# Kernel tuning notes

Measured on AMD Instinct MI355X. Metric: run time of the kernel, lower is better.

## Reference

```python
import jax, jax.numpy as jnp
import numpy as np

K = 20
EPS = 1e-5
NEG_SLOPE = 0.2


def knn(x, k):
    # x: [B, C, N] -> idx [B, N, k] of nearest neighbors (negative sq-dist topk)
    inner = -2.0 * jnp.einsum('bcn,bcm->bnm', x, x)
    xx = jnp.sum(x * x, axis=1)  # [B, N]
    d = -xx[:, :, None] - inner - xx[:, None, :]
    return jax.lax.top_k(d, k)[1]


def get_graph_feature(x, k):
    # x: [B, C, N] -> [B, 2C, N, k]
    idx = knn(x, k)
    xt = jnp.transpose(x, (0, 2, 1))            # [B, N, C]
    feat = jax.vmap(lambda a, i: a[i])(xt, idx)  # [B, N, k, C]
    center = xt[:, :, None, :]
    out = jnp.concatenate([feat - center, jnp.broadcast_to(center, feat.shape)], axis=-1)
    return jnp.transpose(out, (0, 3, 1, 2))


def conv_bn_lrelu(x, w, g, b):
    # 1x1 conv + BatchNorm2d (batch stats, training mode) + LeakyReLU(0.2)
    y = jnp.einsum('oc,bcnk->bonk', w, x)
    mu = jnp.mean(y, axis=(0, 2, 3), keepdims=True)
    var = jnp.mean((y - mu) ** 2, axis=(0, 2, 3), keepdims=True)
    y = (y - mu) * jax.lax.rsqrt(var + EPS)
    y = y * g[None, :, None, None] + b[None, :, None, None]
    return jnp.where(y >= 0, y, NEG_SLOPE * y)


def lrelu(y):
    return jnp.where(y >= 0, y, NEG_SLOPE * y)


def setup_inputs() -> dict:
    key = jax.random.key(0)
    ks = jax.random.split(key, 24)
    B, N = 8, 4096
    d = {}
    d['x'] = jax.random.normal(ks[0], (B, 3, N), dtype=jnp.float32)
    def wconv(k_, o, c):
        return jax.random.normal(k_, (o, c), dtype=jnp.float32) * (1.0 / np.sqrt(c))
    d['w1'] = wconv(ks[1], 32, 6)
    d['g1'] = 1.0 + 0.1 * jax.random.normal(ks[2], (32,), dtype=jnp.float32)
    d['b1'] = 0.1 * jax.random.normal(ks[3], (32,), dtype=jnp.float32)
    d['w2'] = wconv(ks[4], 64, 70)
    d['g2'] = 1.0 + 0.1 * jax.random.normal(ks[5], (64,), dtype=jnp.float32)
    d['b2'] = 0.1 * jax.random.normal(ks[6], (64,), dtype=jnp.float32)
    d['wd1'] = wconv(ks[7], 64, 64)
    d['gd1'] = 1.0 + 0.1 * jax.random.normal(ks[8], (64,), dtype=jnp.float32)
    d['bd1'] = 0.1 * jax.random.normal(ks[9], (64,), dtype=jnp.float32)
    d['wd2'] = wconv(ks[10], 64, 128)
    d['gd2'] = 1.0 + 0.1 * jax.random.normal(ks[11], (64,), dtype=jnp.float32)
    d['bd2'] = 0.1 * jax.random.normal(ks[12], (64,), dtype=jnp.float32)
    d['W2d'] = jax.random.normal(ks[13], (128, 128), dtype=jnp.float32) * (1.0 / np.sqrt(128))
    d['b2d'] = 0.1 * jax.random.normal(ks[14], (128,), dtype=jnp.float32)
    d['W3d'] = jax.random.normal(ks[15], (64, 128), dtype=jnp.float32) * (1.0 / np.sqrt(128))
    d['b3d'] = 0.1 * jax.random.normal(ks[16], (64,), dtype=jnp.float32)
    d['W4d'] = jax.random.normal(ks[17], (11, 64), dtype=jnp.float32) * (1.0 / np.sqrt(64))
    d['b4d'] = 0.1 * jax.random.normal(ks[18], (11,), dtype=jnp.float32)
    return d


def reference(x, w1, g1, b1, w2, g2, b2, wd1, gd1, bd1, wd2, gd2, bd2,
              W2d, b2d, W3d, b3d, W4d, b4d):
    x1_gf = get_graph_feature(x, K)                    # [B, 6, N, k]
    x1_max = jnp.max(conv_bn_lrelu(x1_gf, w1, g1, b1), axis=-1)  # [B, 32, N]
    x2_gf = jnp.concatenate([x1_gf, get_graph_feature(x1_max, K)], axis=1)  # [B, 70, N, k]
    x2_max = jnp.max(conv_bn_lrelu(x2_gf, w2, g2, b2), axis=-1)  # [B, 64, N]
    xd1 = jnp.max(conv_bn_lrelu(get_graph_feature(x1_max, K), wd1, gd1, bd1), axis=-1)  # [B, 64, N]
    xd2 = jnp.max(conv_bn_lrelu(get_graph_feature(x2_max, K), wd2, gd2, bd2), axis=-1)  # [B, 64, N]
    h = jnp.concatenate([xd1, xd2], axis=1)            # [B, 128, N]
    h = h.reshape(1, -1, 128)                          # faithful row-major view
    h = jnp.mean(h, axis=1)                            # [1, 128]
    h = lrelu(h @ W2d.T + b2d)
    h = lrelu(h @ W3d.T + b3d)
    return lrelu(h @ W4d.T + b4d)                      # [1, 11]
```

## Files before the change

### kernel.cpp

```cpp
#include <hip/hip_runtime.h>

#define BB 8
#define NN 4096
#define KK 20
constexpr float EPSV = 1e-5f;
constexpr float SLOPE = 0.2f;

typedef __bf16 bfrag __attribute__((ext_vector_type(8)));
typedef float floatx4 __attribute__((ext_vector_type(4)));
typedef unsigned short us8 __attribute__((ext_vector_type(8)));

__device__ __forceinline__ float lrelu(float v) { return v >= 0.f ? v : SLOPE * v; }

__device__ __forceinline__ unsigned short bf16rn(float f) {
    unsigned int u = __float_as_uint(f);
    return (unsigned short)((u + 0x7FFFu + ((u >> 16) & 1u)) >> 16);
}
__device__ __forceinline__ float bf16up(unsigned short h) {
    return __uint_as_float(((unsigned int)h) << 16);
}

__device__ __forceinline__ void gl2lds16(const void* g, void* l) {
    __builtin_amdgcn_global_load_lds(
        (const __attribute__((address_space(1))) unsigned int*)g,
        (__attribute__((address_space(3))) unsigned int*)l, 16, 0, 0);
}

__global__ void zero_kernel(float* p, int n) {
    int i = blockIdx.x * 256 + threadIdx.x;
    if (i < n) p[i] = 0.f;
}

template<int C>
__global__ void halfnorm_kernel(const float* __restrict__ src, float* __restrict__ hng) {
    int n = blockIdx.x * 256 + threadIdx.x;
    int b = blockIdx.y;
    float s = 0.f;
    #pragma unroll
    for (int c = 0; c < C; c++) { float v = src[(b * C + c) * NN + n]; s += v * v; }
    hng[b * NN + n] = 0.5f * s;
}

template<int C>
__global__ void pack_kernel(const float* __restrict__ src, unsigned short* __restrict__ pk) {
    constexpr int NCH = C / 4;
    int i = blockIdx.x * 256 + threadIdx.x;
    int b = blockIdx.y;
    int n = i / NCH, j = i % NCH;
    us8 v;
    if (j < C / 8) {
        int c0 = j * 8;
        #pragma unroll
        for (int cc = 0; cc < 8; cc++)
            v[cc] = bf16rn(src[(b * C + c0 + cc) * NN + n]);
    } else {
        int c0 = (j - C / 8) * 8;
        #pragma unroll
        for (int cc = 0; cc < 8; cc++) {
            float f = src[(b * C + c0 + cc) * NN + n];
            unsigned short h = bf16rn(f);
            v[cc] = bf16rn(f - bf16up(h));
        }
    }
    int phys = j ^ (n & (NCH - 1));
    *(us8*)(pk + ((size_t)(b * NN + n) * NCH + phys) * 8) = v;
}

__global__ void pack3_kernel(const float* __restrict__ src,
                             unsigned short* __restrict__ pa, unsigned short* __restrict__ pb) {
    int n = blockIdx.x * 256 + threadIdx.x;
    int b = blockIdx.y;
    unsigned short h[3], l[3];
    #pragma unroll
    for (int c = 0; c < 3; c++) {
        float f = src[(b * 3 + c) * NN + n];
        h[c] = bf16rn(f);
        l[c] = bf16rn(f - bf16up(h[c]));
    }
    unsigned short A[32], B[32];
    #pragma unroll
    for (int k = 0; k < 32; k++) { A[k] = 0; B[k] = 0; }
    #pragma unroll
    for (int c = 0; c < 3; c++) {
        A[c] = h[c];     A[3 + c] = l[c];  A[6 + c] = h[c];  A[9 + c] = l[c];
        B[c] = h[c];     B[3 + c] = l[c];  B[6 + c] = l[c];  B[9 + c] = h[c];
    }
    size_t base = (size_t)(b * NN + n) * 32;
    #pragma unroll
    for (int j = 0; j < 4; j++) {
        int phys = j ^ (n & 3);
        us8 va, vb;
        #pragma unroll
        for (int t = 0; t < 8; t++) { va[t] = A[j * 8 + t]; vb[t] = B[j * 8 + t]; }
        *(us8*)(pa + base + phys * 8) = va;
        *(us8*)(pb + base + phys * 8) = vb;
    }
}

template<int C>
__global__ __launch_bounds__(256) void knn_kernel(const unsigned short* __restrict__ pq,
                                                  const unsigned short* __restrict__ pc,
                                                  const float* __restrict__ hng,
                                                  int* __restrict__ idx) {
    constexpr int RS = (C == 3) ? 32 : 2 * C;
    constexpr int NCHR = RS / 8;
    constexpr int SWM = NCHR - 1;
    __shared__ unsigned short qpack[64 * RS];
    __shared__ unsigned short cpack[128 * RS];
    __shared__ float hn[128];
    __shared__ float pv[64 * 33];
    __shared__ unsigned short pidx[64 * 34];
    __shared__ float tau[64];
    __shared__ int   cnt[64];

    const int b = blockIdx.y;
    const int q0 = blockIdx.x * 64;
    const int tid = threadIdx.x;
    const int lane = tid & 63;
    const int wv = tid >> 6;
    const int fl = lane & 15;
    const int fq = lane >> 4;
    const int wr = (wv >> 1) * 32;
    const int wc = (wv & 1) * 64;

    {
        const char* gq = (const char*)(pq + (size_t)(b * NN + q0) * RS);
        constexpr int PQW = (64 * RS * 2 / 1024) / 4;
        #pragma unroll
        for (int t = 0; t < PQW; t++) {
            int seg = wv * PQW + t;
            gl2lds16(gq + seg * 1024 + lane * 16, (char*)qpack + seg * 1024);
        }
    }
    if (tid < 64) { tau[tid] = -3.4e38f; cnt[tid] = 0; }

    float tv[20]; int ti[20];
    #pragma unroll
    for (int k = 0; k < 20; k++) { tv[k] = -3.4e38f; ti[k] = 0; }

    for (int ch = 0; ch < 32; ch++) {
        const int m0 = ch * 128;
        {
            const char* gc = (const char*)(pc + (size_t)(b * NN + m0) * RS);
            constexpr int PCW = (128 * RS * 2 / 1024) / 4;
            #pragma unroll
            for (int t = 0; t < PCW; t++) {
                int seg = wv * PCW + t;
                gl2lds16(gc + seg * 1024 + lane * 16, (char*)cpack + seg * 1024);
            }
        }
        if (tid < 128) hn[tid] = hng[b * NN + m0 + tid];
        __syncthreads();

        floatx4 acc[2][4];
        #pragma unroll
        for (int r2 = 0; r2 < 2; r2++)
            #pragma unroll
            for (int c2 = 0; c2 < 4; c2++)
                acc[r2][c2] = (floatx4)(0.f);

        if constexpr (C == 3) {
            bfrag a[2];
            #pragma unroll
            for (int r2 = 0; r2 < 2; r2++) {
                int row = wr + r2 * 16 + fl;
                a[r2] = *(const bfrag*)(qpack + row * RS + (fq ^ (row & SWM)) * 8);
            }
            #pragma unroll
            for (int c2 = 0; c2 < 4; c2++) {
                int row = wc + c2 * 16 + fl;
                bfrag bm = *(const bfrag*)(cpack + row * RS + (fq ^ (row & SWM)) * 8);
                #pragma unroll
                for (int r2 = 0; r2 < 2; r2++)
                    acc[r2][c2] = __builtin_amdgcn_mfma_f32_16x16x32_bf16(a[r2], bm, acc[r2][c2], 0, 0, 0);
            }
        } else {
            #pragma unroll
            for (int kk = 0; kk < C / 32; kk++) {
                bfrag ah[2], al[2], bh[4], bl[4];
                #pragma unroll
                for (int r2 = 0; r2 < 2; r2++) {
                    int row = wr + r2 * 16 + fl;
                    ah[r2] = *(const bfrag*)(qpack + row * RS + ((kk * 4 + fq) ^ (row & SWM)) * 8);
                    al[r2] = *(const bfrag*)(qpack + row * RS + ((C / 8 + kk * 4 + fq) ^ (row & SWM)) * 8);
                }
                #pragma unroll
                for (int c2 = 0; c2 < 4; c2++) {
                    int row = wc + c2 * 16 + fl;
                    bh[c2] = *(const bfrag*)(cpack + row * RS + ((kk * 4 + fq) ^ (row & SWM)) * 8);
                    bl[c2] = *(const bfrag*)(cpack + row * RS + ((C / 8 + kk * 4 + fq) ^ (row & SWM)) * 8);
                }
                #pragma unroll
                for (int r2 = 0; r2 < 2; r2++)
                    #pragma unroll
                    for (int c2 = 0; c2 < 4; c2++) {
                        acc[r2][c2] = __builtin_amdgcn_mfma_f32_16x16x32_bf16(ah[r2], bh[c2], acc[r2][c2], 0, 0, 0);
                        acc[r2][c2] = __builtin_amdgcn_mfma_f32_16x16x32_bf16(ah[r2], bl[c2], acc[r2][c2], 0, 0, 0);
                        acc[r2][c2] = __builtin_amdgcn_mfma_f32_16x16x32_bf16(al[r2], bh[c2], acc[r2][c2], 0, 0, 0);
                        acc[r2][c2] = __builtin_amdgcn_mfma_f32_16x16x32_bf16(al[r2], bl[c2], acc[r2][c2], 0, 0, 0);
                    }
            }
        }

        auto filter_one = [&](int c2) {
            float hnv = hn[wc + c2 * 16 + fl];
            #pragma unroll
            for (int r2 = 0; r2 < 2; r2++) {
                const float* tp = &tau[wr + r2 * 16 + fq * 4];
                float t0 = tp[0], t1 = tp[1], t2 = tp[2], t3 = tp[3];
                float ta[4] = {t0, t1, t2, t3};
                #pragma unroll
                for (int reg = 0; reg < 4; reg++) {
                    float s = acc[r2][c2][reg] - hnv;
                    if (s > ta[reg]) {
                        int q = wr + r2 * 16 + fq * 4 + reg;
                        int p = atomicAdd(&cnt[q], 1);
                        if (p < 32) {
                            pv[q * 33 + p] = s;
                            pidx[q * 34 + p] = (unsigned short)(m0 + wc + c2 * 16 + fl);
                        }
                    }
                }
            }
        };
        auto drain = [&]() {
            if (lane < 16) {
                int qd = wv * 16 + lane;
                int n = cnt[qd]; if (n > 32) n = 32;
                for (int t = 0; t < n; t++) {
                    float v = pv[qd * 33 + t];
                    if (v > tv[0]) {
                        tv[0] = v; ti[0] = (int)pidx[qd * 34 + t];
                        #pragma unroll
                        for (int j = 0; j < 19; j++) {
                            if (tv[j] > tv[j + 1]) {
                                float a = tv[j]; tv[j] = tv[j + 1]; tv[j + 1] = a;
                                int bi = ti[j]; ti[j] = ti[j + 1]; ti[j + 1] = bi;
                            }
                        }
                    }
                }
                cnt[qd] = 0;
                tau[qd] = tv[0];
            }
        };

        if (ch == 0) {
            #pragma unroll
            for (int ph = 0; ph < 4; ph++) {
                filter_one(ph);
                __syncthreads();
                drain();
                __syncthreads();
            }
        } else {
            #pragma unroll
            for (int c2 = 0; c2 < 4; c2++) filter_one(c2);
            __syncthreads();
            drain();
        }
    }

    if (lane < 16) {
        int q = q0 + wv * 16 + lane;
        #pragma unroll
        for (int k = 0; k < 20; k++)
            idx[(b * NN + q) * KK + k] = ti[k];
    }
}

template<int COUT>
__global__ void precompute_kernel(const float* __restrict__ src, int C,
                                  const float* __restrict__ w, int CIN, int wd_off, int wc_off,
                                  float* __restrict__ G, float* __restrict__ H,
                                  int initG, int initH) {
    constexpr int MY = 256 / COUT;
    extern __shared__ float lds[];
    float* wd = lds;
    float* wc = lds + C * COUT;
    const int b = blockIdx.y;
    const int tid = threadIdx.y * COUT + threadIdx.x;
    for (int i = tid; i < C * COUT; i += 256) {
        int c = i / COUT, o = i % COUT;
        float a  = w[o * CIN + wd_off + c];
        float cc = w[o * CIN + wc_off + c];
        wd[i] = a;
        wc[i] = cc - a;
    }
    __syncthreads();
    const int o = threadIdx.x;
    for (int it = 0; it < COUT / 4; it++) {
        int m = blockIdx.x * 64 + it * MY + threadIdx.y;
        float g = 0.f, h = 0.f;
        for (int c = 0; c < C; c++) {
            float s = src[(b * C + c) * NN + m];
            g += wd[c * COUT + o] * s;
            h += wc[c * COUT + o] * s;
        }
        int gi = (b * NN + m) * COUT + o;
        if (initG) G[gi] = g; else G[gi] += g;
        if (initH) H[gi] = h; else H[gi] += h;
    }
}

template<int COUT, int GROUPS>
__global__ void conv_stats_kernel(const float* __restrict__ G1, const int* __restrict__ idx1,
                                  const float* __restrict__ G2, const int* __restrict__ idx2,
                                  const float* __restrict__ H, float* __restrict__ stats,
                                  float* __restrict__ MaxY, float* __restrict__ MinY) {
    constexpr int NY = 256 / COUT;
    const int b = blockIdx.y;
    const int o = threadIdx.x;
    const int n = blockIdx.x * NY + threadIdx.y;
    const int base = b * NN + n;
    const float h = H[base * COUT + o];
    float s1 = 0.f, s2 = 0.f;
    float gx = -3.4e38f, gn = 3.4e38f;
    #pragma unroll
    for (int k = 0; k < KK; k++) {
        int i1 = idx1[base * KK + k];
        float g = G1[(b * NN + i1) * COUT + o];
        if (GROUPS == 2) {
            int i2 = idx2[base * KK + k];
            g += G2[(b * NN + i2) * COUT + o];
        }
        float y = g + h;
        s1 += y;
        s2 += y * y;
        gx = fmaxf(gx, g);
        gn = fminf(gn, g);
    }
    MaxY[base * COUT + o] = gx + h;
    MinY[base * COUT + o] = gn + h;

    __shared__ float ls[2 * COUT];
    if (threadIdx.y == 0) { ls[o] = 0.f; ls[COUT + o] = 0.f; }
    __syncthreads();
    atomicAdd(&ls[o], s1);
    atomicAdd(&ls[COUT + o], s2);
    __syncthreads();
    if (threadIdx.y == 0) {
        atomicAdd(&stats[o], ls[o]);
        atomicAdd(&stats[64 + o], ls[COUT + o]);
    }
}

__global__ void finalize_kernel(const float* __restrict__ g, const float* __restrict__ bb,
                                float* __restrict__ stats, int cout, float invP) {
    int o = threadIdx.x;
    if (o >= cout) return;
    float mu  = stats[o] * invP;
    float var = stats[64 + o] * invP - mu * mu;
    float sc  = g[o] * rsqrtf(var + EPSV);
    stats[128 + o] = sc;
    stats[192 + o] = bb[o] - mu * sc;
}

__global__ void apply_kernel(const float* __restrict__ MaxY, const float* __restrict__ MinY,
                             const float* __restrict__ stats, float* __restrict__ out, int cout) {
    int e = blockIdx.x * 256 + threadIdx.x;
    int total = BB * cout * NN;
    if (e >= total) return;
    int n = e & (NN - 1);
    int o = (e >> 12) % cout;
    int b = e / (NN * cout);
    float sc = stats[128 + o], sh = stats[192 + o];
    int si = (b * NN + n) * cout + o;
    float v = (sc >= 0.f) ? MaxY[si] : MinY[si];
    out[e] = lrelu(sc * v + sh);
}

__global__ void mean_kernel(const float* __restrict__ xd1, const float* __restrict__ xd2,
                            float* __restrict__ hsum) {
    __shared__ float bins[128];
    const int tid = threadIdx.x;
    if (tid < 128) bins[tid] = 0.f;
    __syncthreads();
    const int half = BB * 64 * NN;
    const int stride = gridDim.x * 256;
    for (int e = blockIdx.x * 256 + tid; e < half; e += stride)
        atomicAdd(&bins[e & 127], xd1[e]);
    for (int e = blockIdx.x * 256 + tid; e < half; e += stride)
        atomicAdd(&bins[e & 127], xd2[e]);
    __syncthreads();
    if (tid < 128) atomicAdd(&hsum[tid], bins[tid]);
}

__global__ void head_kernel(const float* __restrict__ hsum,
                            const float* __restrict__ W2d, const float* __restrict__ b2d,
                            const float* __restrict__ W3d, const float* __restrict__ b3d,
                            const float* __restrict__ W4d, const float* __restrict__ b4d,
                            float* __restrict__ out) {
    __shared__ float h[128], t1[128], t2[64];
    const int t = threadIdx.x;
    h[t] = hsum[t] * (1.f / 32768.f);
    __syncthreads();
    float a = b2d[t];
    for (int j = 0; j < 128; j++) a += W2d[t * 128 + j] * h[j];
    t1[t] = lrelu(a);
    __syncthreads();
    if (t < 64) {
        float a2 = b3d[t];
        for (int j = 0; j < 128; j++) a2 += W3d[t * 128 + j] * t1[j];
        t2[t] = lrelu(a2);
    }
    __syncthreads();
    if (t < 11) {
        float a3 = b4d[t];
        for (int j = 0; j < 64; j++) a3 += W4d[t * 64 + j] * t2[j];
        out[t] = lrelu(a3);
    }
}

extern "C" void kernel_launch(void* const* d_in, const int* in_sizes, int n_in,
                              void* d_out, int out_size, void* d_ws, size_t ws_size,
                              hipStream_t stream) {
    const float* x   = (const float*)d_in[0];
    const float* w1  = (const float*)d_in[1];
    const float* g1  = (const float*)d_in[2];
    const float* b1  = (const float*)d_in[3];
    const float* w2  = (const float*)d_in[4];
    const float* g2  = (const float*)d_in[5];
    const float* b2  = (const float*)d_in[6];
    const float* wd1 = (const float*)d_in[7];
    const float* gd1 = (const float*)d_in[8];
    const float* bd1 = (const float*)d_in[9];
    const float* wd2 = (const float*)d_in[10];
    const float* gd2 = (const float*)d_in[11];
    const float* bd2 = (const float*)d_in[12];
    const float* W2d = (const float*)d_in[13];
    const float* b2d = (const float*)d_in[14];
    const float* W3d = (const float*)d_in[15];
    const float* b3d = (const float*)d_in[16];
    const float* W4d = (const float*)d_in[17];
    const float* b4d = (const float*)d_in[18];
    float* out = (float*)d_out;

    char* ws = (char*)d_ws;
    size_t off = 0;
    auto alloc = [&](size_t bytes) { char* p = ws + off; off += (bytes + 255) & ~size_t(255); return p; };
    int*   idx1  = (int*)  alloc(BB * NN * KK * 4);
    int*   idx2  = (int*)  alloc(BB * NN * KK * 4);
    int*   idx3  = (int*)  alloc(BB * NN * KK * 4);
    float* x1m   = (float*)alloc(BB * 32 * NN * 4);
    float* x2m   = (float*)alloc(BB * 64 * NN * 4);
    float* xd1   = (float*)alloc(BB * 64 * NN * 4);
    float* xd2   = (float*)alloc(BB * 64 * NN * 4);
    float* G1    = (float*)alloc((size_t)BB * NN * 64 * 4);
    float* G2    = (float*)alloc((size_t)BB * NN * 64 * 4);
    float* H     = (float*)alloc((size_t)BB * NN * 64 * 4);
    float* MaxY  = (float*)alloc((size_t)BB * NN * 64 * 4);
    float* MinY  = (float*)alloc((size_t)BB * NN * 64 * 4);
    float* stats = (float*)alloc(256 * 4);
    float* hsum  = (float*)alloc(128 * 4);
    float* hng   = (float*)alloc(BB * NN * 4);
    unsigned short* pa3  = (unsigned short*)alloc((size_t)BB * NN * 32 * 2);
    unsigned short* pb3  = (unsigned short*)alloc((size_t)BB * NN * 32 * 2);
    unsigned short* pk32 = (unsigned short*)alloc((size_t)BB * NN * 64 * 2);
    unsigned short* pk64 = (unsigned short*)alloc((size_t)BB * NN * 128 * 2);

    const float invP = 1.f / (float)(BB * NN * KK);
    const dim3 knn_grid(NN / 64, BB);
    const dim3 hn_grid(NN / 256, BB);

    zero_kernel<<<1, 256, 0, stream>>>(hsum, 128);

    halfnorm_kernel<3><<<hn_grid, 256, 0, stream>>>(x, hng);
    pack3_kernel<<<dim3(NN / 256, BB), 256, 0, stream>>>(x, pa3, pb3);
    knn_kernel<3><<<knn_grid, 256, 0, stream>>>(pa3, pb3, hng, idx1);

    zero_kernel<<<1, 256, 0, stream>>>(stats, 128);
    precompute_kernel<32><<<dim3(NN / 64, BB), dim3(32, 8), 2 * 3 * 32 * 4, stream>>>(
        x, 3, w1, 6, 0, 3, G1, H, 1, 1);
    conv_stats_kernel<32, 1><<<dim3(NN / 8, BB), dim3(32, 8), 0, stream>>>(
        G1, idx1, nullptr, nullptr, H, stats, MaxY, MinY);
    finalize_kernel<<<1, 64, 0, stream>>>(g1, b1, stats, 32, invP);
    apply_kernel<<<(BB * 32 * NN + 255) / 256, 256, 0, stream>>>(MaxY, MinY, stats, x1m, 32);

    halfnorm_kernel<32><<<hn_grid, 256, 0, stream>>>(x1m, hng);
    pack_kernel<32><<<dim3(NN * 8 / 256, BB), 256, 0, stream>>>(x1m, pk32);
    knn_kernel<32><<<knn_grid, 256, 0, stream>>>(pk32, pk32, hng, idx2);

    zero_kernel<<<1, 256, 0, stream>>>(stats, 128);
    precompute_kernel<64><<<dim3(NN / 64, BB), dim3(64, 4), 2 * 3 * 64 * 4, stream>>>(
        x, 3, w2, 70, 0, 3, G1, H, 1, 1);
    precompute_kernel<64><<<dim3(NN / 64, BB), dim3(64, 4), 2 * 32 * 64 * 4, stream>>>(
        x1m, 32, w2, 70, 6, 38, G2, H, 1, 0);
    conv_stats_kernel<64, 2><<<dim3(NN / 4, BB), dim3(64, 4), 0, stream>>>(
        G1, idx1, G2, idx2, H, stats, MaxY, MinY);
    finalize_kernel<<<1, 64, 0, stream>>>(g2, b2, stats, 64, invP);
    apply_kernel<<<(BB * 64 * NN + 255) / 256, 256, 0, stream>>>(MaxY, MinY, stats, x2m, 64);

    zero_kernel<<<1, 256, 0, stream>>>(stats, 128);
    precompute_kernel<64><<<dim3(NN / 64, BB), dim3(64, 4), 2 * 32 * 64 * 4, stream>>>(
        x1m, 32, wd1, 64, 0, 32, G1, H, 1, 1);
    conv_stats_kernel<64, 1><<<dim3(NN / 4, BB), dim3(64, 4), 0, stream>>>(
        G1, idx2, nullptr, nullptr, H, stats, MaxY, MinY);
    finalize_kernel<<<1, 64, 0, stream>>>(gd1, bd1, stats, 64, invP);
    apply_kernel<<<(BB * 64 * NN + 255) / 256, 256, 0, stream>>>(MaxY, MinY, stats, xd1, 64);

    halfnorm_kernel<64><<<hn_grid, 256, 0, stream>>>(x2m, hng);
    pack_kernel<64><<<dim3(NN * 16 / 256, BB), 256, 0, stream>>>(x2m, pk64);
    knn_kernel<64><<<knn_grid, 256, 0, stream>>>(pk64, pk64, hng, idx3);

    zero_kernel<<<1, 256, 0, stream>>>(stats, 128);
    precompute_kernel<64><<<dim3(NN / 64, BB), dim3(64, 4), 2 * 64 * 64 * 4, stream>>>(
        x2m, 64, wd2, 128, 0, 64, G1, H, 1, 1);
    conv_stats_kernel<64, 1><<<dim3(NN / 4, BB), dim3(64, 4), 0, stream>>>(
        G1, idx3, nullptr, nullptr, H, stats, MaxY, MinY);
    finalize_kernel<<<1, 64, 0, stream>>>(gd2, bd2, stats, 64, invP);
    apply_kernel<<<(BB * 64 * NN + 255) / 256, 256, 0, stream>>>(MaxY, MinY, stats, xd2, 64);

    mean_kernel<<<1024, 256, 0, stream>>>(xd1, xd2, hsum);
    head_kernel<<<1, 128, 0, stream>>>(hsum, W2d, b2d, W3d, b3d, W4d, b4d, out);
}
```

Before: 1.791 ms.

## Rework KNN candidate filtering with larger buffer and retry rounds; fold zeroing into kernels

The KNN filter now uses a 56-entry per-query candidate buffer, compares against the live tau in LDS, and retries dropped candidates in rounds until no block thread overflows, with the final drain deferred to the end. This replaces the fixed four-phase filter/drain with its extra barriers on the first chunk. The standalone zero kernels are removed: stats zeroing moves into precompute_kernel and the mean reduction writes per-block partials that head_kernel sums, dropping several tiny launches and global atomics. The round loop adds a barrier-count reduction per chunk and more LDS use, which may lower occupancy.

```diff
diff --git a/kernel.cpp b/kernel.cpp
--- a/kernel.cpp
+++ b/kernel.cpp
@@ -24,11 +24,6 @@
     __builtin_amdgcn_global_load_lds(
         (const __attribute__((address_space(1))) unsigned int*)g,
         (__attribute__((address_space(3))) unsigned int*)l, 16, 0, 0);
-}
-
-__global__ void zero_kernel(float* p, int n) {
-    int i = blockIdx.x * 256 + threadIdx.x;
-    if (i < n) p[i] = 0.f;
 }
 
 template<int C>
@@ -103,13 +98,13 @@
                                                   const float* __restrict__ hng,
                                                   int* __restrict__ idx) {
     constexpr int RS = (C == 3) ? 32 : 2 * C;
-    constexpr int NCHR = RS / 8;
-    constexpr int SWM = NCHR - 1;
+    constexpr int SWM = RS / 8 - 1;
+    constexpr int CAPL = 56;
     __shared__ unsigned short qpack[64 * RS];
     __shared__ unsigned short cpack[128 * RS];
     __shared__ float hn[128];
-    __shared__ float pv[64 * 33];
-    __shared__ unsigned short pidx[64 * 34];
+    __shared__ float pv[64 * (CAPL + 1)];
+    __shared__ unsigned short pidx[64 * (CAPL + 2)];
     __shared__ float tau[64];
     __shared__ int   cnt[64];
 
@@ -202,35 +197,44 @@
             }
         }
 
-        auto filter_one = [&](int c2) {
-            float hnv = hn[wc + c2 * 16 + fl];
+        unsigned int done = 0u;
+        for (int round = 0; round < 8; round++) {
+            bool dropped = false;
             #pragma unroll
-            for (int r2 = 0; r2 < 2; r2++) {
-                const float* tp = &tau[wr + r2 * 16 + fq * 4];
-                float t0 = tp[0], t1 = tp[1], t2 = tp[2], t3 = tp[3];
-                float ta[4] = {t0, t1, t2, t3};
+            for (int c2 = 0; c2 < 4; c2++) {
+                float hnv = hn[wc + c2 * 16 + fl];
                 #pragma unroll
-                for (int reg = 0; reg < 4; reg++) {
-                    float s = acc[r2][c2][reg] - hnv;
-                    if (s > ta[reg]) {
-                        int q = wr + r2 * 16 + fq * 4 + reg;
-                        int p = atomicAdd(&cnt[q], 1);
-                        if (p < 32) {
-                            pv[q * 33 + p] = s;
-                            pidx[q * 34 + p] = (unsigned short)(m0 + wc + c2 * 16 + fl);
+                for (int r2 = 0; r2 < 2; r2++) {
+                    #pragma unroll
+                    for (int reg = 0; reg < 4; reg++) {
+                        unsigned int bit = 1u << ((c2 << 3) | (r2 << 2) | reg);
+                        if (!(done & bit)) {
+                            int q = wr + r2 * 16 + fq * 4 + reg;
+                            float s = acc[r2][c2][reg] - hnv;
+                            if (s > tau[q]) {
+                                int p = atomicAdd(&cnt[q], 1);
+                                if (p < CAPL) {
+                                    pv[q * (CAPL + 1) + p] = s;
+                                    pidx[q * (CAPL + 2) + p] = (unsigned short)(m0 + wc + c2 * 16 + fl);
+                                    done |= bit;
+                                } else {
+                                    dropped = true;
+                                }
+                            } else {
+                                done |= bit;
+                            }
                         }
                     }
                 }
             }
-        };
-        auto drain = [&]() {
+            if (__syncthreads_count(dropped ? 1 : 0) == 0) break;
             if (lane < 16) {
                 int qd = wv * 16 + lane;
-                int n = cnt[qd]; if (n > 32) n = 32;
+                int n = cnt[qd]; if (n > CAPL) n = CAPL;
                 for (int t = 0; t < n; t++) {
-                    float v = pv[qd * 33 + t];
+                    float v = pv[qd * (CAPL + 1) + t];
                     if (v > tv[0]) {
-                        tv[0] = v; ti[0] = (int)pidx[qd * 34 + t];
+                        tv[0] = v; ti[0] = (int)pidx[qd * (CAPL + 2) + t];
                         #pragma unroll
                         for (int j = 0; j < 19; j++) {
                             if (tv[j] > tv[j + 1]) {
@@ -243,26 +247,27 @@
                 cnt[qd] = 0;
                 tau[qd] = tv[0];
             }
-        };
-
-        if (ch == 0) {
-            #pragma unroll
-            for (int ph = 0; ph < 4; ph++) {
-                filter_one(ph);
-                __syncthreads();
-                drain();
-                __syncthreads();
-            }
-        } else {
-            #pragma unroll
-            for (int c2 = 0; c2 < 4; c2++) filter_one(c2);
             __syncthreads();
-            drain();
         }
     }
 
     if (lane < 16) {
-        int q = q0 + wv * 16 + lane;
+        int qd = wv * 16 + lane;
+        int n = cnt[qd]; if (n > CAPL) n = CAPL;
+        for (int t = 0; t < n; t++) {
+            float v = pv[qd * (CAPL + 1) + t];
+            if (v > tv[0]) {
+                tv[0] = v; ti[0] = (int)pidx[qd * (CAPL + 2) + t];
+                #pragma unroll
+                for (int j = 0; j < 19; j++) {
+                    if (tv[j] > tv[j + 1]) {
+                        float a = tv[j]; tv[j] = tv[j + 1]; tv[j + 1] = a;
+                        int bi = ti[j]; ti[j] = ti[j + 1]; ti[j + 1] = bi;
+                    }
+                }
+            }
+        }
+        int q = q0 + qd;
         #pragma unroll
         for (int k = 0; k < 20; k++)
             idx[(b * NN + q) * KK + k] = ti[k];
@@ -273,13 +278,14 @@
 __global__ void precompute_kernel(const float* __restrict__ src, int C,
                                   const float* __restrict__ w, int CIN, int wd_off, int wc_off,
                                   float* __restrict__ G, float* __restrict__ H,
-                                  int initG, int initH) {
+                                  int initG, int initH, float* __restrict__ stats, int zero_stats) {
     constexpr int MY = 256 / COUT;
     extern __shared__ float lds[];
     float* wd = lds;
     float* wc = lds + C * COUT;
     const int b = blockIdx.y;
     const int tid = threadIdx.y * COUT + threadIdx.x;
+    if (zero_stats && blockIdx.x == 0 && blockIdx.y == 0 && tid < 128) stats[tid] = 0.f;
     for (int i = tid; i < C * COUT; i += 256) {
         int c = i / COUT, o = i % COUT;
         float a  = w[o * CIN + wd_off + c];
@@ -371,7 +377,7 @@
 }
 
 __global__ void mean_kernel(const float* __restrict__ xd1, const float* __restrict__ xd2,
-                            float* __restrict__ hsum) {
+                            float* __restrict__ hpart) {
     __shared__ float bins[128];
     const int tid = threadIdx.x;
     if (tid < 128) bins[tid] = 0.f;
@@ -383,17 +389,19 @@
     for (int e = blockIdx.x * 256 + tid; e < half; e += stride)
         atomicAdd(&bins[e & 127], xd2[e]);
     __syncthreads();
-    if (tid < 128) atomicAdd(&hsum[tid], bins[tid]);
-}
-
-__global__ void head_kernel(const float* __restrict__ hsum,
+    if (tid < 128) hpart[blockIdx.x * 128 + tid] = bins[tid];
+}
+
+__global__ void head_kernel(const float* __restrict__ hpart, int nparts,
                             const float* __restrict__ W2d, const float* __restrict__ b2d,
                             const float* __restrict__ W3d, const float* __restrict__ b3d,
                             const float* __restrict__ W4d, const float* __restrict__ b4d,
                             float* __restrict__ out) {
     __shared__ float h[128], t1[128], t2[64];
     const int t = threadIdx.x;
-    h[t] = hsum[t] * (1.f / 32768.f);
+    float s = 0.f;
+    for (int j = 0; j < nparts; j++) s += hpart[j * 128 + t];
+    h[t] = s * (1.f / 32768.f);
     __syncthreads();
     float a = b2d[t];
     for (int j = 0; j < 128; j++) a += W2d[t * 128 + j] * h[j];
@@ -452,7 +460,7 @@
     float* MaxY  = (float*)alloc((size_t)BB * NN * 64 * 4);
     float* MinY  = (float*)alloc((size_t)BB * NN * 64 * 4);
     float* stats = (float*)alloc(256 * 4);
-    float* hsum  = (float*)alloc(128 * 4);
+    float* hpart = (float*)alloc(128 * 128 * 4);
     float* hng   = (float*)alloc(BB * NN * 4);
     unsigned short* pa3  = (unsigned short*)alloc((size_t)BB * NN * 32 * 2);
     unsigned short* pb3  = (unsigned short*)alloc((size_t)BB * NN * 32 * 2);
@@ -463,15 +471,12 @@
     const dim3 knn_grid(NN / 64, BB);
     const dim3 hn_grid(NN / 256, BB);
 
-    zero_kernel<<<1, 256, 0, stream>>>(hsum, 128);
-
     halfnorm_kernel<3><<<hn_grid, 256, 0, stream>>>(x, hng);
     pack3_kernel<<<dim3(NN / 256, BB), 256, 0, stream>>>(x, pa3, pb3);
     knn_kernel<3><<<knn_grid, 256, 0, stream>>>(pa3, pb3, hng, idx1);
 
-    zero_kernel<<<1, 256, 0, stream>>>(stats, 128);
     precompute_kernel<32><<<dim3(NN / 64, BB), dim3(32, 8), 2 * 3 * 32 * 4, stream>>>(
-        x, 3, w1, 6, 0, 3, G1, H, 1, 1);
+        x, 3, w1, 6, 0, 3, G1, H, 1, 1, stats, 1);
     conv_stats_kernel<32, 1><<<dim3(NN / 8, BB), dim3(32, 8), 0, stream>>>(
         G1, idx1, nullptr, nullptr, H, stats, MaxY, MinY);
     finalize_kernel<<<1, 64, 0, stream>>>(g1, b1, stats, 32, invP);
@@ -481,19 +486,17 @@
     pack_kernel<32><<<dim3(NN * 8 / 256, BB), 256, 0, stream>>>(x1m, pk32);
     knn_kernel<32><<<knn_grid, 256, 0, stream>>>(pk32, pk32, hng, idx2);
 
-    zero_kernel<<<1, 256, 0, stream>>>(stats, 128);
     precompute_kernel<64><<<dim3(NN / 64, BB), dim3(64, 4), 2 * 3 * 64 * 4, stream>>>(
-        x, 3, w2, 70, 0, 3, G1, H, 1, 1);
+        x, 3, w2, 70, 0, 3, G1, H, 1, 1, stats, 1);
     precompute_kernel<64><<<dim3(NN / 64, BB), dim3(64, 4), 2 * 32 * 64 * 4, stream>>>(
-        x1m, 32, w2, 70, 6, 38, G2, H, 1, 0);
+        x1m, 32, w2, 70, 6, 38, G2, H, 1, 0, stats, 0);
     conv_stats_kernel<64, 2><<<dim3(NN / 4, BB), dim3(64, 4), 0, stream>>>(
         G1, idx1, G2, idx2, H, stats, MaxY, MinY);
     finalize_kernel<<<1, 64, 0, stream>>>(g2, b2, stats, 64, invP);
     apply_kernel<<<(BB * 64 * NN + 255) / 256, 256, 0, stream>>>(MaxY, MinY, stats, x2m, 64);
 
-    zero_kernel<<<1, 256, 0, stream>>>(stats, 128);
     precompute_kernel<64><<<dim3(NN / 64, BB), dim3(64, 4), 2 * 32 * 64 * 4, stream>>>(
-        x1m, 32, wd1, 64, 0, 32, G1, H, 1, 1);
+        x1m, 32, wd1, 64, 0, 32, G1, H, 1, 1, stats, 1);
     conv_stats_kernel<64, 1><<<dim3(NN / 4, BB), dim3(64, 4), 0, stream>>>(
         G1, idx2, nullptr, nullptr, H, stats, MaxY, MinY);
     finalize_kernel<<<1, 64, 0, stream>>>(gd1, bd1, stats, 64, invP);
@@ -503,14 +506,13 @@
     pack_kernel<64><<<dim3(NN * 16 / 256, BB), 256, 0, stream>>>(x2m, pk64);
     knn_kernel<64><<<knn_grid, 256, 0, stream>>>(pk64, pk64, hng, idx3);
 
-    zero_kernel<<<1, 256, 0, stream>>>(stats, 128);
     precompute_kernel<64><<<dim3(NN / 64, BB), dim3(64, 4), 2 * 64 * 64 * 4, stream>>>(
-        x2m, 64, wd2, 128, 0, 64, G1, H, 1, 1);
+        x2m, 64, wd2, 128, 0, 64, G1, H, 1, 1, stats, 1);
     conv_stats_kernel<64, 1><<<dim3(NN / 4, BB), dim3(64, 4), 0, stream>>>(
         G1, idx3, nullptr, nullptr, H, stats, MaxY, MinY);
     finalize_kernel<<<1, 64, 0, stream>>>(gd2, bd2, stats, 64, invP);
     apply_kernel<<<(BB * 64 * NN + 255) / 256, 256, 0, stream>>>(MaxY, MinY, stats, xd2, 64);
 
-    mean_kernel<<<1024, 256, 0, stream>>>(xd1, xd2, hsum);
-    head_kernel<<<1, 128, 0, stream>>>(hsum, W2d, b2d, W3d, b3d, W4d, b4d, out);
-}
+    mean_kernel<<<128, 256, 0, stream>>>(xd1, xd2, hpart);
+    head_kernel<<<1, 128, 0, stream>>>(hpart, 128, W2d, b2d, W3d, b3d, W4d, b4d, out);
+}
```

New measurement: 2.352 ms. 31.3% more time.
